# Kernel tuning notes

Hardware: AMD Instinct MI355X
Metric: run time of the kernel (lower is better)

## Reference

```python
import jax, jax.numpy as jnp
import numpy as np

V, E, H, K, B, T = 50000, 128, 256, 9, 128, 512
HD = H // 2  # hidden per direction


def setup_inputs() -> dict:
    key = jax.random.key(0)
    ks = jax.random.split(key, 16)
    s = 0.1
    inp = {
        "x": jax.random.randint(ks[0], (B, T), 0, V),
        "emb": jax.random.normal(ks[1], (V, E), jnp.float32) * 0.02,
        "w_ih_f": jax.random.normal(ks[2], (4 * HD, E), jnp.float32) * s,
        "w_hh_f": jax.random.normal(ks[3], (4 * HD, HD), jnp.float32) * s,
        "b_ih_f": jax.random.normal(ks[4], (4 * HD,), jnp.float32) * s,
        "b_hh_f": jax.random.normal(ks[5], (4 * HD,), jnp.float32) * s,
        "w_ih_b": jax.random.normal(ks[6], (4 * HD, E), jnp.float32) * s,
        "w_hh_b": jax.random.normal(ks[7], (4 * HD, HD), jnp.float32) * s,
        "b_ih_b": jax.random.normal(ks[8], (4 * HD,), jnp.float32) * s,
        "b_hh_b": jax.random.normal(ks[9], (4 * HD,), jnp.float32) * s,
        "W_tag": jax.random.normal(ks[10], (K, H), jnp.float32) * s,
        "b_tag": jax.random.normal(ks[11], (K,), jnp.float32) * s,
        "start_trans": jax.random.normal(ks[12], (K,), jnp.float32) * s,
        "end_trans": jax.random.normal(ks[13], (K,), jnp.float32) * s,
        "trans": jax.random.normal(ks[14], (K, K), jnp.float32) * s,
    }
    return inp


def _lstm_dir(xs, w_ih, w_hh, b_ih, b_hh, reverse):
    # xs: [T, B, E]; PyTorch gate order: i, f, g, o
    Bsz = xs.shape[1]
    hd = w_hh.shape[1]
    b = b_ih + b_hh

    def step(carry, x_t):
        h, c = carry
        gates = x_t @ w_ih.T + h @ w_hh.T + b  # [B, 4*hd]
        i, f, g, o = jnp.split(gates, 4, axis=-1)
        i = jax.nn.sigmoid(i)
        f = jax.nn.sigmoid(f)
        g = jnp.tanh(g)
        o = jax.nn.sigmoid(o)
        c = f * c + i * g
        h = o * jnp.tanh(c)
        return (h, c), h

    init = (jnp.zeros((Bsz, hd), xs.dtype), jnp.zeros((Bsz, hd), xs.dtype))
    _, hs = jax.lax.scan(step, init, xs, reverse=reverse)
    return hs  # [T, B, hd], time-ordered


def _viterbi(emissions, start_trans, end_trans, trans):
    # emissions: [T, B, K]; returns best tag path [B, T] (torchcrf decode, no mask)
    score0 = start_trans[None, :] + emissions[0]  # [B, K]

    def step(score, emis_t):
        # score[b, i] + trans[i, j] -> best over i
        cand = score[:, :, None] + trans[None, :, :]  # [B, K, K]
        bp = jnp.argmax(cand, axis=1)                 # [B, K] best prev tag
        best = jnp.max(cand, axis=1)
        return best + emis_t, bp

    final_score, bps = jax.lax.scan(step, score0, emissions[1:])  # bps: [T-1, B, K]
    final_score = final_score + end_trans[None, :]
    last_tag = jnp.argmax(final_score, axis=-1)  # [B]

    def back(tag, bp):
        prev = jnp.take_along_axis(bp, tag[:, None], axis=1)[:, 0]
        return prev, prev

    _, path = jax.lax.scan(back, last_tag, bps, reverse=True)  # [T-1, B]
    tags = jnp.concatenate([path, last_tag[None, :]], axis=0)  # [T, B]
    return tags.T.astype(jnp.int32)  # [B, T]


def reference(x, emb, w_ih_f, w_hh_f, b_ih_f, b_hh_f,
              w_ih_b, w_hh_b, b_ih_b, b_hh_b,
              W_tag, b_tag, start_trans, end_trans, trans):
    xt = x.T                        # [T, B]
    e = emb[xt]                     # [T, B, E] embedding gather
    h_f = _lstm_dir(e, w_ih_f, w_hh_f, b_ih_f, b_hh_f, reverse=False)
    h_b = _lstm_dir(e, w_ih_b, w_hh_b, b_ih_b, b_hh_b, reverse=True)
    h = jnp.concatenate([h_f, h_b], axis=-1)  # [T, B, H]
    # dropout is identity at inference
    emissions = h @ W_tag.T + b_tag           # [T, B, K]
    return _viterbi(emissions, start_trans, end_trans, trans)
```

## Files before the change

kernel.cpp:

```cpp
#include <hip/hip_runtime.h>
#include <math.h>

#define TT 512
#define BB 128
#define KK 9

__device__ __forceinline__ float fast_sigmoid(float x) {
    const float LOG2E = 1.4426950408889634f;
    float e = __builtin_amdgcn_exp2f(-x * LOG2E);
    return __builtin_amdgcn_rcpf(1.0f + e);
}
__device__ __forceinline__ float fast_tanh(float x) {
    const float LOG2E = 1.4426950408889634f;
    float a = fabsf(x);
    float e = __builtin_amdgcn_exp2f(-2.0f * a * LOG2E);
    float t = (1.0f - e) * __builtin_amdgcn_rcpf(1.0f + e);
    return copysignf(t, x);
}

__global__ __launch_bounds__(256, 3) void input_gemm(
    const int* __restrict__ x, const float* __restrict__ emb,
    const float* __restrict__ w_ih_f, const float* __restrict__ w_ih_b,
    const float* __restrict__ b_ih_f, const float* __restrict__ b_hh_f,
    const float* __restrict__ b_ih_b, const float* __restrict__ b_hh_b,
    float* __restrict__ buf_f, float* __restrict__ buf_b,
    int t0f, int t0b)
{
    const int dir = blockIdx.z;
    const int s   = blockIdx.x;
    const int n0  = blockIdx.y * 128;
    const int t   = (dir ? t0b : t0f) + s;
    const float* w  = dir ? w_ih_b : w_ih_f;
    const float* bi = dir ? b_ih_b : b_ih_f;
    const float* bh = dir ? b_hh_b : b_hh_f;
    float* dst = dir ? buf_b : buf_f;

    __shared__ __align__(16) float As[32][132];
    __shared__ __align__(16) float Bs[32][132];

    const int tid  = threadIdx.x;
    const int lrow = tid >> 3;
    const int k4   = (tid & 7) * 4;

    int tokr[4];
    #pragma unroll
    for (int p = 0; p < 4; p++) tokr[p] = x[(p * 32 + lrow) * TT + t];

    const int tx = tid & 15;
    const int ty = tid >> 4;

    float acc[8][8];
    #pragma unroll
    for (int i = 0; i < 8; i++)
        #pragma unroll
        for (int j = 0; j < 8; j++) acc[i][j] = 0.0f;

    float4 aS[4], bS[4];
    #pragma unroll
    for (int p = 0; p < 4; p++) {
        aS[p] = *(const float4*)(emb + (size_t)tokr[p] * 128 + k4);
        bS[p] = *(const float4*)(w + (size_t)(n0 + p * 32 + lrow) * 128 + k4);
    }

    for (int kc = 0; kc < 128; kc += 32) {
        __syncthreads();
        #pragma unroll
        for (int p = 0; p < 4; p++) {
            const int row = p * 32 + lrow;
            As[k4 + 0][row] = aS[p].x; As[k4 + 1][row] = aS[p].y;
            As[k4 + 2][row] = aS[p].z; As[k4 + 3][row] = aS[p].w;
            Bs[k4 + 0][row] = bS[p].x; Bs[k4 + 1][row] = bS[p].y;
            Bs[k4 + 2][row] = bS[p].z; Bs[k4 + 3][row] = bS[p].w;
        }
        __syncthreads();
        if (kc + 32 < 128) {
            #pragma unroll
            for (int p = 0; p < 4; p++) {
                aS[p] = *(const float4*)(emb + (size_t)tokr[p] * 128 + kc + 32 + k4);
                bS[p] = *(const float4*)(w + (size_t)(n0 + p * 32 + lrow) * 128 + kc + 32 + k4);
            }
        }
        #pragma unroll 8
        for (int k = 0; k < 32; k++) {
            float4 af0 = *(const float4*)&As[k][ty * 8];
            float4 af1 = *(const float4*)&As[k][ty * 8 + 4];
            float4 bf0 = *(const float4*)&Bs[k][tx * 8];
            float4 bf1 = *(const float4*)&Bs[k][tx * 8 + 4];
            float a_[8] = {af0.x, af0.y, af0.z, af0.w, af1.x, af1.y, af1.z, af1.w};
            float b_[8] = {bf0.x, bf0.y, bf0.z, bf0.w, bf1.x, bf1.y, bf1.z, bf1.w};
            #pragma unroll
            for (int i = 0; i < 8; i++)
                #pragma unroll
                for (int j = 0; j < 8; j++)
                    acc[i][j] += a_[i] * b_[j];
        }
    }

    const int nbase = n0 + tx * 8;
    float bias[8];
    #pragma unroll
    for (int j = 0; j < 8; j++) {
        int n = nbase + j;
        bias[j] = bi[n] + bh[n];
    }
    #pragma unroll
    for (int i = 0; i < 8; i++) {
        int brow = ty * 8 + i;
        float* o = dst + ((size_t)s * 128 + brow) * 512 + nbase;
        float4 v0, v1;
        v0.x = acc[i][0] + bias[0]; v0.y = acc[i][1] + bias[1];
        v0.z = acc[i][2] + bias[2]; v0.w = acc[i][3] + bias[3];
        v1.x = acc[i][4] + bias[4]; v1.y = acc[i][5] + bias[5];
        v1.z = acc[i][6] + bias[6]; v1.w = acc[i][7] + bias[7];
        *(float4*)o = v0;
        *(float4*)(o + 4) = v1;
    }
}

__global__ __launch_bounds__(512, 2) void lstm_chunk(
    const float* __restrict__ buf_f, const float* __restrict__ buf_b,
    const float* __restrict__ w_hh_f, const float* __restrict__ w_hh_b,
    float* __restrict__ h_all,
    float* __restrict__ h_state, float* __restrict__ c_state,
    int t0f, int t0b, int C, int init)
{
    const int dir = blockIdx.x >> 7;
    const int b   = blockIdx.x & 127;
    const int j   = threadIdx.x;
    const int w_  = j >> 6;
    const int l   = j & 63;
    const int m   = l >> 2;
    const int q   = l & 3;
    const int k   = w_ * 16 + m;
    const int r   = q * 128 + k;

    const float* whh = dir ? w_hh_b : w_hh_f;
    float wR[128];
    #pragma unroll
    for (int qq = 0; qq < 32; qq++) {
        float4 v = *(const float4*)(whh + (size_t)r * 128 + qq * 4);
        wR[4*qq+0] = v.x; wR[4*qq+1] = v.y; wR[4*qq+2] = v.z; wR[4*qq+3] = v.w;
    }

    __shared__ __align__(16) float h_lds[2][128];
    float c;
    if (init) {
        c = 0.0f;
        if (q == 0) h_lds[0][k] = 0.0f;
    } else {
        c = c_state[((size_t)dir * 128 + b) * 128 + k];
        if (q == 0) h_lds[0][k] = h_state[((size_t)dir * 128 + b) * 128 + k];
    }
    __syncthreads();

    const float* buf = dir ? buf_b : buf_f;
    const int t0     = dir ? t0b : t0f;
    const int  tl0   = dir ? (C - 1) : 0;
    const long lstep = dir ? -(long)(128 * 512) : (long)(128 * 512);

    const float* xp = buf + ((size_t)tl0 * 128 + b) * 512 + r;
    float xw = *xp;
    float h_reg = 0.0f;

    for (int s = 0; s < C; s++) {
        const int t = t0 + (dir ? (C - 1 - s) : s);
        const int p = s & 1;
        const float* hprev = h_lds[p];

        float a0 = 0.f, a1 = 0.f, a2 = 0.f, a3 = 0.f;
        #pragma unroll
        for (int qq = 0; qq < 32; qq++) {
            float4 h4 = *(const float4*)&hprev[4 * qq];
            a0 += wR[4*qq+0] * h4.x;
            a1 += wR[4*qq+1] * h4.y;
            a2 += wR[4*qq+2] * h4.z;
            a3 += wR[4*qq+3] * h4.w;
        }
        float pre = xw + ((a0 + a1) + (a2 + a3));

        float act = (q == 2) ? fast_tanh(pre) : fast_sigmoid(pre);

        float f_ = __shfl_xor(act, 1);
        float g_ = __shfl_xor(act, 2);
        float o_ = __shfl_xor(act, 3);

        c = f_ * c + act * g_;
        h_reg = o_ * fast_tanh(c);
        if (q == 0) h_lds[p ^ 1][k] = h_reg;

        __syncthreads();

        if (s + 1 < C) { xp += lstep; xw = *xp; }
        if (q == 0)
            h_all[((size_t)t * BB + b) * 256 + dir * 128 + k] = h_reg;
    }

    if (q == 0) {
        h_state[((size_t)dir * 128 + b) * 128 + k] = h_reg;
        c_state[((size_t)dir * 128 + b) * 128 + k] = c;
    }
}

__global__ __launch_bounds__(256) void emis_kernel(
    const float* __restrict__ h_all, const float* __restrict__ W_tag,
    const float* __restrict__ b_tag, float* __restrict__ em_sum)
{
    const int wid  = threadIdx.x >> 6;
    const int lane = threadIdx.x & 63;
    const size_t m = (size_t)blockIdx.x * 4 + wid;
    const float4 hv = *(const float4*)(h_all + m * 256 + lane * 4);
    #pragma unroll
    for (int kk = 0; kk < KK; kk++) {
        const float4 wv = *(const float4*)(W_tag + kk * 256 + lane * 4);
        float p = hv.x * wv.x + hv.y * wv.y + hv.z * wv.z + hv.w * wv.w;
        #pragma unroll
        for (int off = 32; off > 0; off >>= 1) p += __shfl_down(p, off);
        if (lane == 0) em_sum[m * KK + kk] = p + b_tag[kk];
    }
}

__device__ __forceinline__ void vmax(float va, int ia, float vb, int ib,
                                     float& vo, int& io) {
    bool gt = vb > va;
    vo = gt ? vb : va;
    io = gt ? ib : ia;
}

__global__ __launch_bounds__(64) void viterbi_kernel(
    const float* __restrict__ em_sum,
    const float* __restrict__ start_trans, const float* __restrict__ end_trans,
    const float* __restrict__ trans, int* __restrict__ out)
{
    const int b = blockIdx.x;
    const int lane = threadIdx.x;
    __shared__ float em_s[TT * KK];
    __shared__ unsigned char bp[TT][KK];

    for (int f = lane; f < TT * KK; f += 64) {
        int t = f / KK, kk = f - t * KK;
        em_s[f] = em_sum[((size_t)t * BB + b) * KK + kk];
    }
    __syncthreads();

    float trans_col[KK];
    float score = -1e30f;
    if (lane < KK) {
        #pragma unroll
        for (int i = 0; i < KK; i++) trans_col[i] = trans[i * KK + lane];
        score = start_trans[lane] + em_s[lane];
    }

    float em_cur = (lane < KK) ? em_s[KK + lane] : 0.0f;
    for (int t = 1; t < TT; t++) {
        float em_next = (t + 1 < TT && lane < KK) ? em_s[(t + 1) * KK + lane] : 0.0f;

        float my = (lane < KK) ? score : -1e30f;
        float cand[KK];
        #pragma unroll
        for (int i = 0; i < KK; i++) cand[i] = __shfl(my, i) + trans_col[i];

        float v01, v23, v45, v67, v03, v47, v07, vb_;
        int   i01, i23, i45, i67, i03, i47, i07, ib_;
        vmax(cand[0], 0, cand[1], 1, v01, i01);
        vmax(cand[2], 2, cand[3], 3, v23, i23);
        vmax(cand[4], 4, cand[5], 5, v45, i45);
        vmax(cand[6], 6, cand[7], 7, v67, i67);
        vmax(v01, i01, v23, i23, v03, i03);
        vmax(v45, i45, v67, i67, v47, i47);
        vmax(v03, i03, v47, i47, v07, i07);
        vmax(v07, i07, cand[8], 8, vb_, ib_);

        if (lane < KK) {
            bp[t][lane] = (unsigned char)ib_;
            score = vb_ + em_cur;
        }
        em_cur = em_next;
    }

    float fin = (lane < KK) ? (score + end_trans[lane]) : -1e30f;
    float farr[KK];
    #pragma unroll
    for (int jx = 0; jx < KK; jx++) farr[jx] = __shfl(fin, jx);
    float v01, v23, v45, v67, v03, v47, v07, vb_;
    int   i01, i23, i45, i67, i03, i47, i07, bj;
    vmax(farr[0], 0, farr[1], 1, v01, i01);
    vmax(farr[2], 2, farr[3], 3, v23, i23);
    vmax(farr[4], 4, farr[5], 5, v45, i45);
    vmax(farr[6], 6, farr[7], 7, v67, i67);
    vmax(v01, i01, v23, i23, v03, i03);
    vmax(v45, i45, v67, i67, v47, i47);
    vmax(v03, i03, v47, i47, v07, i07);
    vmax(v07, i07, farr[8], 8, vb_, bj);

    if (lane == 0) {
        int tag = bj;
        out[b * TT + (TT - 1)] = tag;
        for (int t = TT - 1; t >= 1; t--) {
            tag = bp[t][tag];
            out[b * TT + t - 1] = tag;
        }
    }
}

extern "C" void kernel_launch(void* const* d_in, const int* in_sizes, int n_in,
                              void* d_out, int out_size, void* d_ws, size_t ws_size,
                              hipStream_t stream)
{
    const int*   x       = (const int*)  d_in[0];
    const float* emb     = (const float*)d_in[1];
    const float* w_ih_f  = (const float*)d_in[2];
    const float* w_hh_f  = (const float*)d_in[3];
    const float* b_ih_f  = (const float*)d_in[4];
    const float* b_hh_f  = (const float*)d_in[5];
    const float* w_ih_b  = (const float*)d_in[6];
    const float* w_hh_b  = (const float*)d_in[7];
    const float* b_ih_b  = (const float*)d_in[8];
    const float* b_hh_b  = (const float*)d_in[9];
    const float* W_tag   = (const float*)d_in[10];
    const float* b_tag   = (const float*)d_in[11];
    const float* start_t = (const float*)d_in[12];
    const float* end_t   = (const float*)d_in[13];
    const float* trans   = (const float*)d_in[14];
    int* out = (int*)d_out;

    const size_t hall_elems  = (size_t)TT * BB * 256;
    const size_t em_elems    = (size_t)TT * BB * KK;
    const size_t state_elems = (size_t)2 * 128 * 128;

    int C = 32;
    const int cands[5] = {512, 256, 128, 64, 32};
    for (int ci = 0; ci < 5; ci++) {
        size_t need = ((size_t)2 * cands[ci] * BB * 512
                       + hall_elems + em_elems
                       + 2 * state_elems) * sizeof(float);
        if (ws_size >= need) { C = cands[ci]; break; }
    }

    float* buf_f   = (float*)d_ws;
    float* buf_b   = buf_f + (size_t)C * BB * 512;
    float* em_sum  = buf_b + (size_t)C * BB * 512;
    float* h_state = em_sum + em_elems;
    float* c_state = h_state + state_elems;
    float* h_all   = c_state + state_elems;

    const int rounds = TT / C;
    for (int r = 0; r < rounds; r++) {
        const int t0f = r * C;
        const int t0b = TT - (r + 1) * C;
        dim3 gg(C, 4, 2);
        input_gemm<<<gg, dim3(256), 0, stream>>>(
            x, emb, w_ih_f, w_ih_b, b_ih_f, b_hh_f, b_ih_b, b_hh_b,
            buf_f, buf_b, t0f, t0b);
        lstm_chunk<<<dim3(256), dim3(512), 0, stream>>>(
            buf_f, buf_b, w_hh_f, w_hh_b, h_all,
            h_state, c_state, t0f, t0b, C, (r == 0) ? 1 : 0);
    }
    emis_kernel<<<dim3((TT * BB) / 4), dim3(256), 0, stream>>>(
        h_all, W_tag, b_tag, em_sum);
    viterbi_kernel<<<dim3(BB), dim3(64), 0, stream>>>(
        em_sum, start_t, end_t, trans, out);
}
```

Baseline: 896.8 us.

## Fuse emission projection and Viterbi decode into final LSTM chunk kernel

Removes the separate emission and Viterbi kernels and does that work in the tail of the last LSTM chunk launch. Each block projects its direction's hidden states onto the tag weights, one row per thread. The backward-direction block publishes partial emissions to global memory and bumps a per-batch flag. The forward-direction block spins on that flag, adds the partials, and runs Viterbi with backtracking. This saves two kernel launches and the full emission round-trip. The cost is an inter-block spin-wait that relies on both blocks of a batch being co-resident, plus extra shared memory in the LSTM kernel that may reduce occupancy.

```diff
diff --git a/kernel.cpp b/kernel.cpp
--- a/kernel.cpp
+++ b/kernel.cpp
@@ -117,12 +117,17 @@
     }
 }
 
-__global__ __launch_bounds__(512, 2) void lstm_chunk(
+__global__ __launch_bounds__(512, 2) void lstm_fused(
     const float* __restrict__ buf_f, const float* __restrict__ buf_b,
     const float* __restrict__ w_hh_f, const float* __restrict__ w_hh_b,
     float* __restrict__ h_all,
     float* __restrict__ h_state, float* __restrict__ c_state,
-    int t0f, int t0b, int C, int init)
+    const float* __restrict__ W_tag, const float* __restrict__ b_tag,
+    const float* __restrict__ start_trans, const float* __restrict__ end_trans,
+    const float* __restrict__ trans,
+    float* __restrict__ emB, unsigned* __restrict__ flags,
+    int* __restrict__ out,
+    int t0f, int t0b, int C, int init, int tail)
 {
     const int dir = blockIdx.x >> 7;
     const int b   = blockIdx.x & 127;
@@ -134,6 +139,10 @@
     const int k   = w_ * 16 + m;
     const int r   = q * 128 + k;
 
+    unsigned snap = 0u;
+    if (tail && dir == 0 && j == 0)
+        snap = __hip_atomic_load(&flags[b], __ATOMIC_RELAXED, __HIP_MEMORY_SCOPE_AGENT);
+
     const float* whh = dir ? w_hh_b : w_hh_f;
     float wR[128];
     #pragma unroll
@@ -199,105 +208,129 @@
         h_state[((size_t)dir * 128 + b) * 128 + k] = h_reg;
         c_state[((size_t)dir * 128 + b) * 128 + k] = c;
     }
-}
-
-__global__ __launch_bounds__(256) void emis_kernel(
-    const float* __restrict__ h_all, const float* __restrict__ W_tag,
-    const float* __restrict__ b_tag, float* __restrict__ em_sum)
-{
-    const int wid  = threadIdx.x >> 6;
-    const int lane = threadIdx.x & 63;
-    const size_t m = (size_t)blockIdx.x * 4 + wid;
-    const float4 hv = *(const float4*)(h_all + m * 256 + lane * 4);
-    #pragma unroll
-    for (int kk = 0; kk < KK; kk++) {
-        const float4 wv = *(const float4*)(W_tag + kk * 256 + lane * 4);
-        float p = hv.x * wv.x + hv.y * wv.y + hv.z * wv.z + hv.w * wv.w;
-        #pragma unroll
-        for (int off = 32; off > 0; off >>= 1) p += __shfl_down(p, off);
-        if (lane == 0) em_sum[m * KK + kk] = p + b_tag[kk];
-    }
-}
-
-__device__ __forceinline__ void vmax(float va, int ia, float vb, int ib,
-                                     float& vo, int& io) {
-    bool gt = vb > va;
-    vo = gt ? vb : va;
-    io = gt ? ib : ia;
-}
-
-__global__ __launch_bounds__(64) void viterbi_kernel(
-    const float* __restrict__ em_sum,
-    const float* __restrict__ start_trans, const float* __restrict__ end_trans,
-    const float* __restrict__ trans, int* __restrict__ out)
-{
-    const int b = blockIdx.x;
-    const int lane = threadIdx.x;
-    __shared__ float em_s[TT * KK];
+
+    if (!tail) return;
+
+    __shared__ __align__(16) float wt_s[KK * 128];
+    __shared__ __align__(16) float em_s[TT * KK];
     __shared__ unsigned char bp[TT][KK];
 
-    for (int f = lane; f < TT * KK; f += 64) {
-        int t = f / KK, kk = f - t * KK;
-        em_s[f] = em_sum[((size_t)t * BB + b) * KK + kk];
-    }
+    for (int f = j; f < KK * 128; f += 512)
+        wt_s[f] = W_tag[(f >> 7) * 256 + dir * 128 + (f & 127)];
     __syncthreads();
 
-    float trans_col[KK];
-    float score = -1e30f;
-    if (lane < KK) {
-        #pragma unroll
-        for (int i = 0; i < KK; i++) trans_col[i] = trans[i * KK + lane];
-        score = start_trans[lane] + em_s[lane];
-    }
-
-    float em_cur = (lane < KK) ? em_s[KK + lane] : 0.0f;
-    for (int t = 1; t < TT; t++) {
-        float em_next = (t + 1 < TT && lane < KK) ? em_s[(t + 1) * KK + lane] : 0.0f;
-
-        float my = (lane < KK) ? score : -1e30f;
-        float cand[KK];
-        #pragma unroll
-        for (int i = 0; i < KK; i++) cand[i] = __shfl(my, i) + trans_col[i];
-
+    {
+        const int t = j;
+        const float* hrow = h_all + ((size_t)t * BB + b) * 256 + dir * 128;
+        float acc[KK];
+        #pragma unroll
+        for (int kk = 0; kk < KK; kk++) acc[kk] = 0.0f;
+        #pragma unroll 4
+        for (int j4 = 0; j4 < 128; j4 += 4) {
+            float4 h4 = *(const float4*)(hrow + j4);
+            #pragma unroll
+            for (int kk = 0; kk < KK; kk++) {
+                float4 wv = *(const float4*)&wt_s[kk * 128 + j4];
+                acc[kk] += h4.x * wv.x + h4.y * wv.y + h4.z * wv.z + h4.w * wv.w;
+            }
+        }
+        if (dir == 1) {
+            float* e = emB + ((size_t)b * TT + t) * KK;
+            #pragma unroll
+            for (int kk = 0; kk < KK; kk++) e[kk] = acc[kk];
+        } else {
+            #pragma unroll
+            for (int kk = 0; kk < KK; kk++)
+                em_s[t * KK + kk] = acc[kk] + b_tag[kk];
+        }
+    }
+
+    if (dir == 1) {
+        __syncthreads();
+        if (j == 0) {
+            __threadfence();
+            __hip_atomic_fetch_add(&flags[b], 1u, __ATOMIC_RELEASE,
+                                   __HIP_MEMORY_SCOPE_AGENT);
+        }
+        return;
+    }
+
+    if (j == 0) {
+        while (__hip_atomic_load(&flags[b], __ATOMIC_ACQUIRE,
+                                 __HIP_MEMORY_SCOPE_AGENT) == snap)
+            __builtin_amdgcn_s_sleep(1);
+    }
+    __syncthreads();
+    for (int f = j; f < TT * KK; f += 512)
+        em_s[f] += emB[(size_t)b * TT * KK + f];
+    __syncthreads();
+
+    if (j < 64) {
+        const int lane = j;
+
+        float trans_col[KK];
+        float score = -1e30f;
+        if (lane < KK) {
+            #pragma unroll
+            for (int i = 0; i < KK; i++) trans_col[i] = trans[i * KK + lane];
+            score = start_trans[lane] + em_s[lane];
+        }
+
+        float em_cur = (lane < KK) ? em_s[KK + lane] : 0.0f;
+        for (int t = 1; t < TT; t++) {
+            float em_next = (t + 1 < TT && lane < KK) ? em_s[(t + 1) * KK + lane] : 0.0f;
+
+            float my = (lane < KK) ? score : -1e30f;
+            float cand[KK];
+            #pragma unroll
+            for (int i = 0; i < KK; i++) cand[i] = __shfl(my, i) + trans_col[i];
+
+            float v01, v23, v45, v67, v03, v47, v07, vb_;
+            int   i01, i23, i45, i67, i03, i47, i07, ib_;
+            {
+                bool gt;
+                gt = cand[1] > cand[0]; v01 = gt ? cand[1] : cand[0]; i01 = gt ? 1 : 0;
+                gt = cand[3] > cand[2]; v23 = gt ? cand[3] : cand[2]; i23 = gt ? 3 : 2;
+                gt = cand[5] > cand[4]; v45 = gt ? cand[5] : cand[4]; i45 = gt ? 5 : 4;
+                gt = cand[7] > cand[6]; v67 = gt ? cand[7] : cand[6]; i67 = gt ? 7 : 6;
+                gt = v23 > v01; v03 = gt ? v23 : v01; i03 = gt ? i23 : i01;
+                gt = v67 > v45; v47 = gt ? v67 : v45; i47 = gt ? i67 : i45;
+                gt = v47 > v03; v07 = gt ? v47 : v03; i07 = gt ? i47 : i03;
+                gt = cand[8] > v07; vb_ = gt ? cand[8] : v07; ib_ = gt ? 8 : i07;
+            }
+
+            if (lane < KK) {
+                bp[t][lane] = (unsigned char)ib_;
+                score = vb_ + em_cur;
+            }
+            em_cur = em_next;
+        }
+
+        float fin = (lane < KK) ? (score + end_trans[lane]) : -1e30f;
+        float farr[KK];
+        #pragma unroll
+        for (int jx = 0; jx < KK; jx++) farr[jx] = __shfl(fin, jx);
         float v01, v23, v45, v67, v03, v47, v07, vb_;
-        int   i01, i23, i45, i67, i03, i47, i07, ib_;
-        vmax(cand[0], 0, cand[1], 1, v01, i01);
-        vmax(cand[2], 2, cand[3], 3, v23, i23);
-        vmax(cand[4], 4, cand[5], 5, v45, i45);
-        vmax(cand[6], 6, cand[7], 7, v67, i67);
-        vmax(v01, i01, v23, i23, v03, i03);
-        vmax(v45, i45, v67, i67, v47, i47);
-        vmax(v03, i03, v47, i47, v07, i07);
-        vmax(v07, i07, cand[8], 8, vb_, ib_);
-
-        if (lane < KK) {
-            bp[t][lane] = (unsigned char)ib_;
-            score = vb_ + em_cur;
-        }
-        em_cur = em_next;
-    }
-
-    float fin = (lane < KK) ? (score + end_trans[lane]) : -1e30f;
-    float farr[KK];
-    #pragma unroll
-    for (int jx = 0; jx < KK; jx++) farr[jx] = __shfl(fin, jx);
-    float v01, v23, v45, v67, v03, v47, v07, vb_;
-    int   i01, i23, i45, i67, i03, i47, i07, bj;
-    vmax(farr[0], 0, farr[1], 1, v01, i01);
-    vmax(farr[2], 2, farr[3], 3, v23, i23);
-    vmax(farr[4], 4, farr[5], 5, v45, i45);
-    vmax(farr[6], 6, farr[7], 7, v67, i67);
-    vmax(v01, i01, v23, i23, v03, i03);
-    vmax(v45, i45, v67, i67, v47, i47);
-    vmax(v03, i03, v47, i47, v07, i07);
-    vmax(v07, i07, farr[8], 8, vb_, bj);
-
-    if (lane == 0) {
-        int tag = bj;
-        out[b * TT + (TT - 1)] = tag;
-        for (int t = TT - 1; t >= 1; t--) {
-            tag = bp[t][tag];
-            out[b * TT + t - 1] = tag;
+        int   i01, i23, i45, i67, i03, i47, i07, bj;
+        {
+            bool gt;
+            gt = farr[1] > farr[0]; v01 = gt ? farr[1] : farr[0]; i01 = gt ? 1 : 0;
+            gt = farr[3] > farr[2]; v23 = gt ? farr[3] : farr[2]; i23 = gt ? 3 : 2;
+            gt = farr[5] > farr[4]; v45 = gt ? farr[5] : farr[4]; i45 = gt ? 5 : 4;
+            gt = farr[7] > farr[6]; v67 = gt ? farr[7] : farr[6]; i67 = gt ? 7 : 6;
+            gt = v23 > v01; v03 = gt ? v23 : v01; i03 = gt ? i23 : i01;
+            gt = v67 > v45; v47 = gt ? v67 : v45; i47 = gt ? i67 : i45;
+            gt = v47 > v03; v07 = gt ? v47 : v03; i07 = gt ? i47 : i03;
+            gt = farr[8] > v07; vb_ = gt ? farr[8] : v07; bj = gt ? 8 : i07;
+        }
+
+        if (lane == 0) {
+            int tag = bj;
+            out[b * TT + (TT - 1)] = tag;
+            for (int t = TT - 1; t >= 1; t--) {
+                tag = bp[t][tag];
+                out[b * TT + t - 1] = tag;
+            }
         }
     }
 }
@@ -324,24 +357,25 @@
     int* out = (int*)d_out;
 
     const size_t hall_elems  = (size_t)TT * BB * 256;
-    const size_t em_elems    = (size_t)TT * BB * KK;
+    const size_t emB_elems   = (size_t)BB * TT * KK;
     const size_t state_elems = (size_t)2 * 128 * 128;
 
     int C = 32;
     const int cands[5] = {512, 256, 128, 64, 32};
     for (int ci = 0; ci < 5; ci++) {
         size_t need = ((size_t)2 * cands[ci] * BB * 512
-                       + hall_elems + em_elems
-                       + 2 * state_elems) * sizeof(float);
+                       + hall_elems + emB_elems
+                       + 2 * state_elems) * sizeof(float) + 512;
         if (ws_size >= need) { C = cands[ci]; break; }
     }
 
     float* buf_f   = (float*)d_ws;
     float* buf_b   = buf_f + (size_t)C * BB * 512;
-    float* em_sum  = buf_b + (size_t)C * BB * 512;
-    float* h_state = em_sum + em_elems;
+    float* emB     = buf_b + (size_t)C * BB * 512;
+    float* h_state = emB + emB_elems;
     float* c_state = h_state + state_elems;
     float* h_all   = c_state + state_elems;
+    unsigned* flags = (unsigned*)(h_all + hall_elems);
 
     const int rounds = TT / C;
     for (int r = 0; r < rounds; r++) {
@@ -351,12 +385,11 @@
         input_gemm<<<gg, dim3(256), 0, stream>>>(
             x, emb, w_ih_f, w_ih_b, b_ih_f, b_hh_f, b_ih_b, b_hh_b,
             buf_f, buf_b, t0f, t0b);
-        lstm_chunk<<<dim3(256), dim3(512), 0, stream>>>(
+        lstm_fused<<<dim3(256), dim3(512), 0, stream>>>(
             buf_f, buf_b, w_hh_f, w_hh_b, h_all,
-            h_state, c_state, t0f, t0b, C, (r == 0) ? 1 : 0);
-    }
-    emis_kernel<<<dim3((TT * BB) / 4), dim3(256), 0, stream>>>(
-        h_all, W_tag, b_tag, em_sum);
-    viterbi_kernel<<<dim3(BB), dim3(64), 0, stream>>>(
-        em_sum, start_t, end_t, trans, out);
-}
+            h_state, c_state,
+            W_tag, b_tag, start_t, end_t, trans,
+            emB, flags, out,
+            t0f, t0b, C, (r == 0) ? 1 : 0, (r == rounds - 1) ? 1 : 0);
+    }
+}
```

Measured after the change: 887.8 us. No clear change (-1.0%).
